# Optimization experiments

Hardware: AMD Instinct MI355X
Metric: run time of the kernel (lower is better)

## Reference

```python
import jax, jax.numpy as jnp
import numpy as np

B, S, D, H = 2, 4096, 512, 8
DK = D // H
LN_EPS = 1e-5


def setup_inputs() -> dict:
    key = jax.random.key(0)
    ks = jax.random.split(key, 12)
    lim = 1.0 / np.sqrt(D)
    inp = {
        "query": jax.random.normal(ks[0], (B, S, D), jnp.float32),
        "key_in": jax.random.normal(ks[1], (B, S, D), jnp.float32),
        "value": jax.random.normal(ks[2], (B, S, D), jnp.float32),
        # causal mask: positions with 0 are masked out (masked_fill(mask == 0, -1e9))
        "mask": jnp.broadcast_to(jnp.tril(jnp.ones((S, S), jnp.int32)), (B, S, S)),
        "Wq": jax.random.uniform(ks[3], (D, D), jnp.float32, -lim, lim),
        "bq": jnp.zeros((D,), jnp.float32),
        "Wk": jax.random.uniform(ks[4], (D, D), jnp.float32, -lim, lim),
        "bk": jnp.zeros((D,), jnp.float32),
        "Wv": jax.random.uniform(ks[5], (D, D), jnp.float32, -lim, lim),
        "bv": jnp.zeros((D,), jnp.float32),
        "Wo": jax.random.uniform(ks[6], (D, D), jnp.float32, -lim, lim),
        "bo": jnp.zeros((D,), jnp.float32),
        "ln_gamma": jnp.ones((D,), jnp.float32),
        "ln_beta": jnp.zeros((D,), jnp.float32),
    }
    return inp


def _split_heads(x):
    # [B, S, D] -> [B, H, S, DK]
    return x.reshape(B, S, H, DK).transpose(0, 2, 1, 3)


def reference(query, key_in, value, mask, Wq, bq, Wk, bk, Wv, bv, Wo, bo, ln_gamma, ln_beta):
    residual = query
    q = _split_heads(query @ Wq.T + bq)
    k = _split_heads(key_in @ Wk.T + bk)
    v = _split_heads(value @ Wv.T + bv)

    scores = jnp.einsum("bhqd,bhkd->bhqk", q, k) / jnp.sqrt(jnp.float32(DK))
    scores = jnp.where(mask[:, None, :, :] == 0, jnp.float32(-1e9), scores)
    attn = jax.nn.softmax(scores, axis=-1)  # dropout is identity in eval mode
    out = jnp.einsum("bhqk,bhkd->bhqd", attn, v)

    out = out.transpose(0, 2, 1, 3).reshape(B, S, D)
    out = out @ Wo.T + bo

    x = out + residual
    mu = jnp.mean(x, axis=-1, keepdims=True)
    var = jnp.mean(jnp.square(x - mu), axis=-1, keepdims=True)
    return (x - mu) * jax.lax.rsqrt(var + LN_EPS) * ln_gamma + ln_beta
```

## Files before the change

### kernel.cpp

```cpp
#include <hip/hip_runtime.h>
#include <hip/hip_bf16.h>

#define B_ 2
#define S_ 4096
#define D_ 512
#define H_ 8
#define DK_ 64

#define SCALE_LOG2 0.1803368801111244f

typedef short short8_t __attribute__((ext_vector_type(8)));
typedef short short4_t __attribute__((ext_vector_type(4)));
typedef float float4_t __attribute__((ext_vector_type(4)));

__device__ __forceinline__ unsigned cvtpk(float a, float b) {
    unsigned r;
    asm("v_cvt_pk_bf16_f32 %0, %1, %2" : "=v"(r) : "v"(a), "v"(b));
    return r;
}
union PU2 { unsigned u[2]; short4_t s4; };
union PU4 { unsigned u[4]; short8_t s8; };

#define MFMA32(a, b, c) __builtin_amdgcn_mfma_f32_16x16x32_bf16((a), (b), (c), 0, 0, 0)

#if __has_builtin(__builtin_amdgcn_mfma_f32_16x16x16bf16_1k)
__device__ __forceinline__ float4_t MFMA16(short4_t a, short4_t b, float4_t c) {
    return __builtin_amdgcn_mfma_f32_16x16x16bf16_1k(a, b, c, 0, 0, 0);
}
#else
__device__ __forceinline__ float4_t MFMA16(short4_t a, short4_t b, float4_t c) {
    asm volatile("v_mfma_f32_16x16x16_bf16 %0, %1, %2, %0" : "+v"(c) : "v"(a), "v"(b));
    return c;
}
#endif

__device__ __forceinline__ void gll16(const void* g, const void* l) {
    __builtin_amdgcn_global_load_lds(
        (__attribute__((address_space(1))) void*)(g),
        (__attribute__((address_space(3))) void*)(l), 16, 0, 0);
}

__global__ __launch_bounds__(256) void convert_all(
    const float* __restrict__ q, const float* __restrict__ k, const float* __restrict__ v,
    const float* __restrict__ Wq, const float* __restrict__ Wk,
    const float* __restrict__ Wv, const float* __restrict__ Wo,
    short* __restrict__ Xq, short* __restrict__ Xk, short* __restrict__ Xv,
    short* __restrict__ Wbf)
{
    const int XN = (B_ * S_ * D_) / 8;
    int gid = blockIdx.x * 256 + threadIdx.x;
    const float* src;
    short8_t* dst;
    int off;
    float sc = 1.f;
    if (gid < 3 * XN) {
        int z = gid >> 19;
        off = gid & (XN - 1);
        src = (z == 0) ? q : (z == 1) ? k : v;
        dst = (short8_t*)((z == 0) ? Xq : (z == 1) ? Xk : Xv);
    } else {
        int g2 = gid - 3 * XN;
        int z = g2 >> 15;
        off = g2 & 32767;
        src = (z == 0) ? Wq : (z == 1) ? Wk : (z == 2) ? Wv : Wo;
        dst = (short8_t*)(Wbf + z * (D_ * D_));
        if (z == 0) sc = SCALE_LOG2;
    }
    float4_t f0 = ((const float4_t*)src)[off * 2] * sc;
    float4_t f1 = ((const float4_t*)src)[off * 2 + 1] * sc;
    PU4 o;
    o.u[0] = cvtpk(f0[0], f0[1]);
    o.u[1] = cvtpk(f0[2], f0[3]);
    o.u[2] = cvtpk(f1[0], f1[1]);
    o.u[3] = cvtpk(f1[2], f1[3]);
    dst[off] = o.s8;
}

__global__ __launch_bounds__(256) void gemm_qkv(
    const short* __restrict__ Xq, const short* __restrict__ Xk, const short* __restrict__ Xv,
    const short* __restrict__ Wbf,
    const float* __restrict__ bq, const float* __restrict__ bk, const float* __restrict__ bv,
    short* __restrict__ Qs, short* __restrict__ Ks, short* __restrict__ Vt)
{
    __shared__ short sA[2][128 * 64];
    __shared__ short sB[2][128 * 64];

    const int z = blockIdx.z;
    const short* X    = (z == 0) ? Xq : (z == 1) ? Xk : Xv;
    const short* W    = Wbf + z * (D_ * D_);
    const float* bias = (z == 0) ? bq : (z == 1) ? bk : bv;

    const int col0 = blockIdx.x * 128, row0 = blockIdx.y * 128;
    const int tid = threadIdx.x, w = tid >> 6, l = tid & 63;
    const int lr = l & 15, lg = l >> 4;
    const int wm = w >> 1, wn = w & 1;
    const int srow = l >> 3, sch = l & 7;

    float4_t acc[4][4];
    #pragma unroll
    for (int i = 0; i < 4; i++)
        #pragma unroll
        for (int j = 0; j < 4; j++)
            acc[i][j] = (float4_t){0.f, 0.f, 0.f, 0.f};

    auto STAGE = [&](int k0, int bi) {
        #pragma unroll
        for (int rnd = 0; rnd < 4; rnd++) {
            int r = rnd * 32 + w * 8 + srow;
            gll16(X + (row0 + r) * D_ + k0 + (sch ^ (r & 7)) * 8, &sA[bi][(rnd * 32 + w * 8) * 64]);
            gll16(W + (col0 + r) * D_ + k0 + (sch ^ (r & 7)) * 8, &sB[bi][(rnd * 32 + w * 8) * 64]);
        }
    };

    STAGE(0, 0);
    for (int ks = 0; ks < 8; ks++) {
        int cur = ks & 1;
        if (ks < 7) {
            STAGE((ks + 1) * 64, cur ^ 1);
            asm volatile("s_waitcnt vmcnt(8)" ::: "memory");
        } else {
            asm volatile("s_waitcnt vmcnt(0)" ::: "memory");
        }
        __builtin_amdgcn_s_barrier();
        __builtin_amdgcn_sched_barrier(0);

        const short* pA = sA[cur];
        const short* pB = sB[cur];
        short8_t a[4], bb[4];
        #pragma unroll
        for (int kk = 0; kk < 2; kk++) {
            #pragma unroll
            for (int i = 0; i < 4; i++) {
                int rw = wm * 64 + i * 16 + lr;
                a[i] = *(const short8_t*)(&pA[rw * 64 + (((kk * 4 + lg) ^ (lr & 7)) * 8)]);
            }
            #pragma unroll
            for (int j = 0; j < 4; j++) {
                int rw = wn * 64 + j * 16 + lr;
                bb[j] = *(const short8_t*)(&pB[rw * 64 + (((kk * 4 + lg) ^ (lr & 7)) * 8)]);
            }
            if (z < 2) {
                #pragma unroll
                for (int i = 0; i < 4; i++)
                    #pragma unroll
                    for (int j = 0; j < 4; j++)
                        acc[i][j] = MFMA32(bb[j], a[i], acc[i][j]);
            } else {
                #pragma unroll
                for (int i = 0; i < 4; i++)
                    #pragma unroll
                    for (int j = 0; j < 4; j++)
                        acc[i][j] = MFMA32(a[i], bb[j], acc[i][j]);
            }
        }
        __builtin_amdgcn_s_barrier();
        __builtin_amdgcn_sched_barrier(0);
    }

    if (z < 2) {
        short* Out = (z == 0) ? Qs : Ks;
        #pragma unroll
        for (int j = 0; j < 4; j++) {
            int colb = col0 + wn * 64 + j * 16 + lg * 4;
            int h = colb >> 6, dk = colb & 63;
            float4_t b4 = *(const float4_t*)(bias + colb);
            if (z == 0) b4 *= SCALE_LOG2;
            #pragma unroll
            for (int i = 0; i < 4; i++) {
                int s = row0 + wm * 64 + i * 16 + lr;
                PU2 o;
                o.u[0] = cvtpk(acc[i][j][0] + b4[0], acc[i][j][1] + b4[1]);
                o.u[1] = cvtpk(acc[i][j][2] + b4[2], acc[i][j][3] + b4[3]);
                *(short4_t*)(Out + (((s >> 12) * H_ + h) * S_ + (s & 4095)) * 64 + dk) = o.s4;
            }
        }
    } else {
        #pragma unroll
        for (int j = 0; j < 4; j++) {
            int dkg = col0 + wn * 64 + j * 16 + lr;
            int h = dkg >> 6, dk = dkg & 63;
            float bv_ = bias[dkg];
            #pragma unroll
            for (int i = 0; i < 4; i++) {
                int s0 = row0 + wm * 64 + i * 16 + lg * 4;
                PU2 o;
                o.u[0] = cvtpk(acc[i][j][0] + bv_, acc[i][j][1] + bv_);
                o.u[1] = cvtpk(acc[i][j][2] + bv_, acc[i][j][3] + bv_);
                *(short4_t*)(Vt + (((s0 >> 12) * H_ + h) * 64 + dk) * S_ + (s0 & 4095)) = o.s4;
            }
        }
    }
}

__global__ __launch_bounds__(256) void attn_kernel(
    const short* __restrict__ Qs, const short* __restrict__ Ks,
    const short* __restrict__ Vt, short* __restrict__ Og)
{
    __shared__ float smem[8192];
    short* sKb = (short*)smem;
    short* sVb = (short*)smem + 8192;

    const int v = blockIdx.x;
    const int bh = (v & 7) * 2 + ((v >> 3) & 1);
    const int qt = 127 - (v >> 4);
    const int b = bh >> 3, h = bh & 7;
    const int tid = threadIdx.x, w = tid >> 6, l = tid & 63;
    const int lr = l & 15, lg = l >> 4;
    const int qbase = qt * 32;
    const int kvT = qt / 2 + 1;
    const short* Kb = Ks + bh * (S_ * 64);
    const short* Vb = Vt + bh * (64 * S_);
    const short* Qb = Qs + bh * (S_ * 64);
    const int srow = l >> 3, sch = l & 7;
    const short4_t ones = { (short)0x3F80, (short)0x3F80, (short)0x3F80, (short)0x3F80 };

    short8_t qf[2][2];
    #pragma unroll
    for (int qb = 0; qb < 2; qb++)
        #pragma unroll
        for (int kk = 0; kk < 2; kk++)
            qf[qb][kk] = *(const short8_t*)(Qb + (qbase + qb * 16 + lr) * 64 + kk * 32 + lg * 8);

    float m_run[2] = {-1e30f, -1e30f};
    float4_t Lacc[2];
    float4_t O[2][4];
    #pragma unroll
    for (int qb = 0; qb < 2; qb++) {
        Lacc[qb] = (float4_t){0.f, 0.f, 0.f, 0.f};
        #pragma unroll
        for (int nj = 0; nj < 4; nj++)
            O[qb][nj] = (float4_t){0.f, 0.f, 0.f, 0.f};
    }

    auto STAGE = [&](int t, int bi) {
        #pragma unroll
        for (int rnd = 0; rnd < 2; rnd++) {
            int r = rnd * 32 + w * 8 + srow;
            gll16(Kb + (t * 64 + r) * 64 + (sch ^ (r & 7)) * 8, sKb + bi * 4096 + (rnd * 32 + w * 8) * 64);
            gll16(Vb + r * S_ + t * 64 + (sch ^ (r & 7)) * 8,   sVb + bi * 4096 + (rnd * 32 + w * 8) * 64);
        }
    };

    STAGE(0, 0);
    for (int t = 0; t < kvT; t++) {
        int cur = t & 1;
        if (t + 1 < kvT) {
            STAGE(t + 1, cur ^ 1);
            asm volatile("s_waitcnt vmcnt(4)" ::: "memory");
        } else {
            asm volatile("s_waitcnt vmcnt(0)" ::: "memory");
        }
        __builtin_amdgcn_s_barrier();
        __builtin_amdgcn_sched_barrier(0);

        const int kv0 = t * 64 + w * 16;
        if (kv0 <= qbase + 16) {
            const short* K_ = sKb + cur * 4096;
            const short* V_ = sVb + cur * 4096;

            short8_t kf[2];
            #pragma unroll
            for (int kk = 0; kk < 2; kk++)
                kf[kk] = *(const short8_t*)(&K_[(w * 16 + lr) * 64 + (((kk * 4 + lg) ^ (lr & 7)) * 8)]);

            __builtin_amdgcn_s_setprio(1);
            float4_t st0 = (float4_t){0.f, 0.f, 0.f, 0.f}, st1 = st0;
            st0 = MFMA32(kf[0], qf[0][0], st0);
            st1 = MFMA32(kf[0], qf[1][0], st1);
            st0 = MFMA32(kf[1], qf[0][1], st0);
            st1 = MFMA32(kf[1], qf[1][1], st1);
            __builtin_amdgcn_s_setprio(0);

            const bool act0 = (kv0 <= qbase);
            const bool diag0 = (kv0 == qbase);
            const bool diag1 = (kv0 == qbase + 16);
            short4_t pb[2];

            #pragma unroll
            for (int qb = 0; qb < 2; qb++) {
                if (qb == 0 && !act0) continue;
                float4_t sx = qb ? st1 : st0;
                bool dg = qb ? diag1 : diag0;
                float mx = fmaxf(fmaxf(sx[0], sx[1]), fmaxf(sx[2], sx[3]));
                mx = fmaxf(mx, __shfl_xor(mx, 16));
                mx = fmaxf(mx, __shfl_xor(mx, 32));
                if (__any(mx > m_run[qb] + 8.f)) {
                    float mnew = fmaxf(m_run[qb], mx);
                    float al = __builtin_exp2f(m_run[qb] - mnew);
                    m_run[qb] = mnew;
                    #pragma unroll
                    for (int nj = 0; nj < 4; nj++) O[qb][nj] *= al;
                    Lacc[qb] *= al;
                }
                float e[4];
                #pragma unroll
                for (int r = 0; r < 4; r++)
                    e[r] = __builtin_exp2f(sx[r] - m_run[qb]);
                if (dg) {
                    #pragma unroll
                    for (int r = 0; r < 4; r++)
                        if (lg * 4 + r > lr) e[r] = 0.f;
                }
                PU2 pu;
                pu.u[0] = cvtpk(e[0], e[1]);
                pu.u[1] = cvtpk(e[2], e[3]);
                pb[qb] = pu.s4;
            }

            __builtin_amdgcn_s_setprio(1);
            if (act0) Lacc[0] = MFMA16(ones, pb[0], Lacc[0]);
            Lacc[1] = MFMA16(ones, pb[1], Lacc[1]);
            #pragma unroll
            for (int njd = 0; njd < 4; njd++) {
                short4_t va = *(const short4_t*)(
                    &V_[(njd * 16 + lr) * 64 + (((w * 2 + (lg >> 1)) ^ (lr & 7)) * 8) + (lg & 1) * 4]);
                if (act0) O[0][njd] = MFMA16(va, pb[0], O[0][njd]);
                O[1][njd] = MFMA16(va, pb[1], O[1][njd]);
            }
            __builtin_amdgcn_s_setprio(0);
        }
        __builtin_amdgcn_s_barrier();
        __builtin_amdgcn_sched_barrier(0);
    }

    float* sml = smem;
    if (lg == 0) {
        #pragma unroll
        for (int qb = 0; qb < 2; qb++) {
            sml[((w * 2 + qb) * 16 + lr) * 2 + 0] = m_run[qb];
            sml[((w * 2 + qb) * 16 + lr) * 2 + 1] = Lacc[qb][0];
        }
    }
    __syncthreads();
    float fac[2];
    #pragma unroll
    for (int qb = 0; qb < 2; qb++) {
        float mw[4], lw[4];
        #pragma unroll
        for (int ww = 0; ww < 4; ww++) {
            mw[ww] = sml[((ww * 2 + qb) * 16 + lr) * 2 + 0];
            lw[ww] = sml[((ww * 2 + qb) * 16 + lr) * 2 + 1];
        }
        float mmax = fmaxf(fmaxf(mw[0], mw[1]), fmaxf(mw[2], mw[3]));
        float lsum = 0.f;
        #pragma unroll
        for (int ww = 0; ww < 4; ww++) lsum += __builtin_exp2f(mw[ww] - mmax) * lw[ww];
        fac[qb] = __builtin_exp2f(m_run[qb] - mmax) / lsum;
    }
    __syncthreads();
    float* rg = smem + w * 2048;
    #pragma unroll
    for (int qb = 0; qb < 2; qb++) {
        #pragma unroll
        for (int njd = 0; njd < 4; njd++) {
            int row = qb * 16 + lr;
            int c = (njd * 4 + lg) ^ (lr & 7);
            float4_t val = O[qb][njd] * fac[qb];
            *(float4_t*)(rg + row * 64 + c * 4) = val;
        }
    }
    __syncthreads();
    {
        int qq = tid >> 3, a = tid & 7;
        int key = qq & 7;
        float4_t s0 = (float4_t){0.f, 0.f, 0.f, 0.f}, s1 = s0;
        #pragma unroll
        for (int ww = 0; ww < 4; ww++) {
            const float* r_ = smem + ww * 2048 + qq * 64;
            s0 += *(const float4_t*)(r_ + ((a * 2) ^ key) * 4);
            s1 += *(const float4_t*)(r_ + ((a * 2 + 1) ^ key) * 4);
        }
        PU4 o;
        o.u[0] = cvtpk(s0[0], s0[1]);
        o.u[1] = cvtpk(s0[2], s0[3]);
        o.u[2] = cvtpk(s1[0], s1[1]);
        o.u[3] = cvtpk(s1[2], s1[3]);
        *(short8_t*)(Og + (b * S_ + qbase + qq) * D_ + h * 64 + a * 8) = o.s8;
    }
}

__global__ __launch_bounds__(256) void gemm_oproj(
    const short* __restrict__ Ag, const short* __restrict__ Wbf,
    const float* __restrict__ bo, float* __restrict__ Og)
{
    __shared__ short sA[2][128 * 64];
    __shared__ short sB[2][128 * 64];

    const int col0 = blockIdx.x * 128, row0 = blockIdx.y * 128;
    const int tid = threadIdx.x, w = tid >> 6, l = tid & 63;
    const int lr = l & 15, lg = l >> 4;
    const int wm = w >> 1, wn = w & 1;
    const int srow = l >> 3, sch = l & 7;

    float4_t acc[4][4];
    #pragma unroll
    for (int i = 0; i < 4; i++)
        #pragma unroll
        for (int j = 0; j < 4; j++)
            acc[i][j] = (float4_t){0.f, 0.f, 0.f, 0.f};

    auto STAGE = [&](int k0, int bi) {
        #pragma unroll
        for (int rnd = 0; rnd < 4; rnd++) {
            int r = rnd * 32 + w * 8 + srow;
            gll16(Ag  + (row0 + r) * D_ + k0 + (sch ^ (r & 7)) * 8, &sA[bi][(rnd * 32 + w * 8) * 64]);
            gll16(Wbf + (col0 + r) * D_ + k0 + (sch ^ (r & 7)) * 8, &sB[bi][(rnd * 32 + w * 8) * 64]);
        }
    };

    STAGE(0, 0);
    for (int ks = 0; ks < 8; ks++) {
        int cur = ks & 1;
        if (ks < 7) {
            STAGE((ks + 1) * 64, cur ^ 1);
            asm volatile("s_waitcnt vmcnt(8)" ::: "memory");
        } else {
            asm volatile("s_waitcnt vmcnt(0)" ::: "memory");
        }
        __builtin_amdgcn_s_barrier();
        __builtin_amdgcn_sched_barrier(0);

        const short* pA = sA[cur];
        const short* pB = sB[cur];
        #pragma unroll
        for (int kk = 0; kk < 2; kk++) {
            short8_t a[4], bb[4];
            #pragma unroll
            for (int i = 0; i < 4; i++) {
                int rw = wm * 64 + i * 16 + lr;
                a[i] = *(const short8_t*)(&pA[rw * 64 + (((kk * 4 + lg) ^ (lr & 7)) * 8)]);
            }
            #pragma unroll
            for (int j = 0; j < 4; j++) {
                int rw = wn * 64 + j * 16 + lr;
                bb[j] = *(const short8_t*)(&pB[rw * 64 + (((kk * 4 + lg) ^ (lr & 7)) * 8)]);
            }
            #pragma unroll
            for (int i = 0; i < 4; i++)
                #pragma unroll
                for (int j = 0; j < 4; j++)
                    acc[i][j] = MFMA32(bb[j], a[i], acc[i][j]);
        }
        __builtin_amdgcn_s_barrier();
        __builtin_amdgcn_sched_barrier(0);
    }

    #pragma unroll
    for (int j = 0; j < 4; j++) {
        int colb = col0 + wn * 64 + j * 16 + lg * 4;
        float4_t b4 = *(const float4_t*)(bo + colb);
        #pragma unroll
        for (int i = 0; i < 4; i++) {
            int s = row0 + wm * 64 + i * 16 + lr;
            float4_t o4 = acc[i][j] + b4;
            *(float4_t*)(Og + s * D_ + colb) = o4;
        }
    }
}

__global__ __launch_bounds__(128) void ln_kernel(
    const float* __restrict__ Oin, const float* __restrict__ resid,
    const float* __restrict__ gamma, const float* __restrict__ beta,
    float* __restrict__ out)
{
    __shared__ float red[4];
    const int row = blockIdx.x, tid = threadIdx.x;
    float4_t o  = *(const float4_t*)(Oin   + row * 512 + tid * 4);
    float4_t rq = *(const float4_t*)(resid + row * 512 + tid * 4);
    float4_t x = o + rq;
    float s1 = x[0] + x[1] + x[2] + x[3];
    float s2 = x[0]*x[0] + x[1]*x[1] + x[2]*x[2] + x[3]*x[3];
    #pragma unroll
    for (int m = 1; m < 64; m <<= 1) {
        s1 += __shfl_xor(s1, m, 64);
        s2 += __shfl_xor(s2, m, 64);
    }
    const int wv = tid >> 6;
    if ((tid & 63) == 0) { red[wv * 2] = s1; red[wv * 2 + 1] = s2; }
    __syncthreads();
    s1 = red[0] + red[2];
    s2 = red[1] + red[3];
    float mu  = s1 * (1.f / 512.f);
    float var = s2 * (1.f / 512.f) - mu * mu;
    float rstd = rsqrtf(var + 1e-5f);
    float4_t g  = *(const float4_t*)(gamma + tid * 4);
    float4_t be = *(const float4_t*)(beta  + tid * 4);
    float4_t y;
    #pragma unroll
    for (int c = 0; c < 4; c++) y[c] = (x[c] - mu) * rstd * g[c] + be[c];
    *(float4_t*)(out + row * 512 + tid * 4) = y;
}

extern "C" void kernel_launch(void* const* d_in, const int* in_sizes, int n_in,
                              void* d_out, int out_size, void* d_ws, size_t ws_size,
                              hipStream_t stream) {
    const float* q     = (const float*)d_in[0];
    const float* kin   = (const float*)d_in[1];
    const float* vin   = (const float*)d_in[2];
    const float* Wq    = (const float*)d_in[4];
    const float* bq    = (const float*)d_in[5];
    const float* Wk    = (const float*)d_in[6];
    const float* bk    = (const float*)d_in[7];
    const float* Wv    = (const float*)d_in[8];
    const float* bv    = (const float*)d_in[9];
    const float* Wo    = (const float*)d_in[10];
    const float* bo    = (const float*)d_in[11];
    const float* gamma = (const float*)d_in[12];
    const float* beta  = (const float*)d_in[13];
    float* out = (float*)d_out;

    char* ws = (char*)d_ws;
    short* Wbf  = (short*)(ws);
    short* Xq   = (short*)(ws + 2097152);
    short* Xk   = (short*)(ws + 10485760);
    short* Xv   = (short*)(ws + 18874368);
    short* Qs   = (short*)(ws + 27262976);
    short* Ks   = (short*)(ws + 35651584);
    short* Vt   = (short*)(ws + 44040192);
    short* Attn = (short*)(ws + 18874368);
    float* Oprj = (float*)(ws + 2097152);

    convert_all<<<6656, 256, 0, stream>>>(q, kin, vin, Wq, Wk, Wv, Wo, Xq, Xk, Xv, Wbf);
    gemm_qkv<<<dim3(4, 64, 3), 256, 0, stream>>>(Xq, Xk, Xv, Wbf, bq, bk, bv, Qs, Ks, Vt);
    attn_kernel<<<2048, 256, 0, stream>>>(Qs, Ks, Vt, Attn);
    gemm_oproj<<<dim3(4, 64), 256, 0, stream>>>(Attn, Wbf + 3 * D_ * D_, bo, Oprj);
    ln_kernel<<<8192, 128, 0, stream>>>(Oprj, q, gamma, beta, out);
}
```

Before: 394.8 us.

## Double attention query tile to 64 rows per block to reuse staged K/V

Each attention block now handles 64 query rows (four 16-row sub-blocks) instead of 32, halving the grid to 1024 blocks and halving the K/V tile loads per query row. The causal check moves from per-tile skipping to diagonal handling only on the last KV tile, with each wave skipping the sub-blocks it does not need. The max shuffle reduction now runs only when a rescale may be needed. The epilogue reduction runs in two passes to fit shared memory. In exchange, register pressure rises from the larger O accumulators and there are fewer blocks to fill the GPU.

```diff
diff --git a/kernel.cpp b/kernel.cpp
--- a/kernel.cpp
+++ b/kernel.cpp
@@ -202,30 +202,30 @@
 
     const int v = blockIdx.x;
     const int bh = (v & 7) * 2 + ((v >> 3) & 1);
-    const int qt = 127 - (v >> 4);
+    const int qt = 63 - (v >> 4);
     const int b = bh >> 3, h = bh & 7;
     const int tid = threadIdx.x, w = tid >> 6, l = tid & 63;
     const int lr = l & 15, lg = l >> 4;
-    const int qbase = qt * 32;
-    const int kvT = qt / 2 + 1;
+    const int qbase = qt * 64;
+    const int kvT = qt + 1;
     const short* Kb = Ks + bh * (S_ * 64);
     const short* Vb = Vt + bh * (64 * S_);
     const short* Qb = Qs + bh * (S_ * 64);
     const int srow = l >> 3, sch = l & 7;
     const short4_t ones = { (short)0x3F80, (short)0x3F80, (short)0x3F80, (short)0x3F80 };
 
-    short8_t qf[2][2];
-    #pragma unroll
-    for (int qb = 0; qb < 2; qb++)
+    short8_t qf[4][2];
+    #pragma unroll
+    for (int qb = 0; qb < 4; qb++)
         #pragma unroll
         for (int kk = 0; kk < 2; kk++)
             qf[qb][kk] = *(const short8_t*)(Qb + (qbase + qb * 16 + lr) * 64 + kk * 32 + lg * 8);
 
-    float m_run[2] = {-1e30f, -1e30f};
-    float4_t Lacc[2];
-    float4_t O[2][4];
-    #pragma unroll
-    for (int qb = 0; qb < 2; qb++) {
+    float m_run[4] = {-1e30f, -1e30f, -1e30f, -1e30f};
+    float4_t Lacc[4];
+    float4_t O[4][4];
+    #pragma unroll
+    for (int qb = 0; qb < 4; qb++) {
         Lacc[qb] = (float4_t){0.f, 0.f, 0.f, 0.f};
         #pragma unroll
         for (int nj = 0; nj < 4; nj++)
@@ -253,72 +253,72 @@
         __builtin_amdgcn_s_barrier();
         __builtin_amdgcn_sched_barrier(0);
 
-        const int kv0 = t * 64 + w * 16;
-        if (kv0 <= qbase + 16) {
-            const short* K_ = sKb + cur * 4096;
-            const short* V_ = sVb + cur * 4096;
-
-            short8_t kf[2];
-            #pragma unroll
-            for (int kk = 0; kk < 2; kk++)
-                kf[kk] = *(const short8_t*)(&K_[(w * 16 + lr) * 64 + (((kk * 4 + lg) ^ (lr & 7)) * 8)]);
-
-            __builtin_amdgcn_s_setprio(1);
-            float4_t st0 = (float4_t){0.f, 0.f, 0.f, 0.f}, st1 = st0;
-            st0 = MFMA32(kf[0], qf[0][0], st0);
-            st1 = MFMA32(kf[0], qf[1][0], st1);
-            st0 = MFMA32(kf[1], qf[0][1], st0);
-            st1 = MFMA32(kf[1], qf[1][1], st1);
-            __builtin_amdgcn_s_setprio(0);
-
-            const bool act0 = (kv0 <= qbase);
-            const bool diag0 = (kv0 == qbase);
-            const bool diag1 = (kv0 == qbase + 16);
-            short4_t pb[2];
-
-            #pragma unroll
-            for (int qb = 0; qb < 2; qb++) {
-                if (qb == 0 && !act0) continue;
-                float4_t sx = qb ? st1 : st0;
-                bool dg = qb ? diag1 : diag0;
-                float mx = fmaxf(fmaxf(sx[0], sx[1]), fmaxf(sx[2], sx[3]));
+        const short* K_ = sKb + cur * 4096;
+        const short* V_ = sVb + cur * 4096;
+        const bool lastT = (t == kvT - 1);
+        const int qbS = lastT ? w : 0;
+
+        short8_t kf[2];
+        #pragma unroll
+        for (int kk = 0; kk < 2; kk++)
+            kf[kk] = *(const short8_t*)(&K_[(w * 16 + lr) * 64 + (((kk * 4 + lg) ^ (lr & 7)) * 8)]);
+
+        float4_t st[4];
+        __builtin_amdgcn_s_setprio(1);
+        #pragma unroll
+        for (int qb = 0; qb < 4; qb++) {
+            if (qb < qbS) continue;
+            st[qb] = (float4_t){0.f, 0.f, 0.f, 0.f};
+            st[qb] = MFMA32(kf[0], qf[qb][0], st[qb]);
+            st[qb] = MFMA32(kf[1], qf[qb][1], st[qb]);
+        }
+        __builtin_amdgcn_s_setprio(0);
+
+        short4_t pb[4];
+        #pragma unroll
+        for (int qb = 0; qb < 4; qb++) {
+            if (qb < qbS) continue;
+            float4_t sx = st[qb];
+            float mx = fmaxf(fmaxf(sx[0], sx[1]), fmaxf(sx[2], sx[3]));
+            if (__any(mx > m_run[qb] + 8.f)) {
                 mx = fmaxf(mx, __shfl_xor(mx, 16));
                 mx = fmaxf(mx, __shfl_xor(mx, 32));
-                if (__any(mx > m_run[qb] + 8.f)) {
-                    float mnew = fmaxf(m_run[qb], mx);
-                    float al = __builtin_exp2f(m_run[qb] - mnew);
-                    m_run[qb] = mnew;
-                    #pragma unroll
-                    for (int nj = 0; nj < 4; nj++) O[qb][nj] *= al;
-                    Lacc[qb] *= al;
-                }
-                float e[4];
+                float mnew = fmaxf(m_run[qb], mx);
+                float al = __builtin_exp2f(m_run[qb] - mnew);
+                m_run[qb] = mnew;
+                #pragma unroll
+                for (int nj = 0; nj < 4; nj++) O[qb][nj] *= al;
+                Lacc[qb] *= al;
+            }
+            float e[4];
+            #pragma unroll
+            for (int r = 0; r < 4; r++)
+                e[r] = __builtin_exp2f(sx[r] - m_run[qb]);
+            if (lastT && qb == w) {
                 #pragma unroll
                 for (int r = 0; r < 4; r++)
-                    e[r] = __builtin_exp2f(sx[r] - m_run[qb]);
-                if (dg) {
-                    #pragma unroll
-                    for (int r = 0; r < 4; r++)
-                        if (lg * 4 + r > lr) e[r] = 0.f;
-                }
-                PU2 pu;
-                pu.u[0] = cvtpk(e[0], e[1]);
-                pu.u[1] = cvtpk(e[2], e[3]);
-                pb[qb] = pu.s4;
-            }
-
-            __builtin_amdgcn_s_setprio(1);
-            if (act0) Lacc[0] = MFMA16(ones, pb[0], Lacc[0]);
-            Lacc[1] = MFMA16(ones, pb[1], Lacc[1]);
-            #pragma unroll
-            for (int njd = 0; njd < 4; njd++) {
-                short4_t va = *(const short4_t*)(
-                    &V_[(njd * 16 + lr) * 64 + (((w * 2 + (lg >> 1)) ^ (lr & 7)) * 8) + (lg & 1) * 4]);
-                if (act0) O[0][njd] = MFMA16(va, pb[0], O[0][njd]);
-                O[1][njd] = MFMA16(va, pb[1], O[1][njd]);
-            }
-            __builtin_amdgcn_s_setprio(0);
-        }
+                    if (lg * 4 + r > lr) e[r] = 0.f;
+            }
+            PU2 pu;
+            pu.u[0] = cvtpk(e[0], e[1]);
+            pu.u[1] = cvtpk(e[2], e[3]);
+            pb[qb] = pu.s4;
+        }
+
+        __builtin_amdgcn_s_setprio(1);
+        #pragma unroll
+        for (int qb = 0; qb < 4; qb++)
+            if (qb >= qbS) Lacc[qb] = MFMA16(ones, pb[qb], Lacc[qb]);
+        #pragma unroll
+        for (int njd = 0; njd < 4; njd++) {
+            short4_t va = *(const short4_t*)(
+                &V_[(njd * 16 + lr) * 64 + (((w * 2 + (lg >> 1)) ^ (lr & 7)) * 8) + (lg & 1) * 4]);
+            #pragma unroll
+            for (int qb = 0; qb < 4; qb++)
+                if (qb >= qbS) O[qb][njd] = MFMA16(va, pb[qb], O[qb][njd]);
+        }
+        __builtin_amdgcn_s_setprio(0);
+
         __builtin_amdgcn_s_barrier();
         __builtin_amdgcn_sched_barrier(0);
     }
@@ -326,20 +326,20 @@
     float* sml = smem;
     if (lg == 0) {
         #pragma unroll
-        for (int qb = 0; qb < 2; qb++) {
-            sml[((w * 2 + qb) * 16 + lr) * 2 + 0] = m_run[qb];
-            sml[((w * 2 + qb) * 16 + lr) * 2 + 1] = Lacc[qb][0];
+        for (int qb = 0; qb < 4; qb++) {
+            sml[((w * 4 + qb) * 16 + lr) * 2 + 0] = m_run[qb];
+            sml[((w * 4 + qb) * 16 + lr) * 2 + 1] = Lacc[qb][0];
         }
     }
     __syncthreads();
-    float fac[2];
-    #pragma unroll
-    for (int qb = 0; qb < 2; qb++) {
+    float fac[4];
+    #pragma unroll
+    for (int qb = 0; qb < 4; qb++) {
         float mw[4], lw[4];
         #pragma unroll
         for (int ww = 0; ww < 4; ww++) {
-            mw[ww] = sml[((ww * 2 + qb) * 16 + lr) * 2 + 0];
-            lw[ww] = sml[((ww * 2 + qb) * 16 + lr) * 2 + 1];
+            mw[ww] = sml[((ww * 4 + qb) * 16 + lr) * 2 + 0];
+            lw[ww] = sml[((ww * 4 + qb) * 16 + lr) * 2 + 1];
         }
         float mmax = fmaxf(fmaxf(mw[0], mw[1]), fmaxf(mw[2], mw[3]));
         float lsum = 0.f;
@@ -348,34 +348,38 @@
         fac[qb] = __builtin_exp2f(m_run[qb] - mmax) / lsum;
     }
     __syncthreads();
-    float* rg = smem + w * 2048;
-    #pragma unroll
-    for (int qb = 0; qb < 2; qb++) {
-        #pragma unroll
-        for (int njd = 0; njd < 4; njd++) {
-            int row = qb * 16 + lr;
-            int c = (njd * 4 + lg) ^ (lr & 7);
-            float4_t val = O[qb][njd] * fac[qb];
-            *(float4_t*)(rg + row * 64 + c * 4) = val;
-        }
-    }
-    __syncthreads();
-    {
-        int qq = tid >> 3, a = tid & 7;
-        int key = qq & 7;
-        float4_t s0 = (float4_t){0.f, 0.f, 0.f, 0.f}, s1 = s0;
-        #pragma unroll
-        for (int ww = 0; ww < 4; ww++) {
-            const float* r_ = smem + ww * 2048 + qq * 64;
-            s0 += *(const float4_t*)(r_ + ((a * 2) ^ key) * 4);
-            s1 += *(const float4_t*)(r_ + ((a * 2 + 1) ^ key) * 4);
-        }
-        PU4 o;
-        o.u[0] = cvtpk(s0[0], s0[1]);
-        o.u[1] = cvtpk(s0[2], s0[3]);
-        o.u[2] = cvtpk(s1[0], s1[1]);
-        o.u[3] = cvtpk(s1[2], s1[3]);
-        *(short8_t*)(Og + (b * S_ + qbase + qq) * D_ + h * 64 + a * 8) = o.s8;
+    #pragma unroll
+    for (int pass = 0; pass < 2; pass++) {
+        float* rg = smem + w * 2048;
+        #pragma unroll
+        for (int q2 = 0; q2 < 2; q2++) {
+            int qb = pass * 2 + q2;
+            #pragma unroll
+            for (int njd = 0; njd < 4; njd++) {
+                int row = q2 * 16 + lr;
+                int c = (njd * 4 + lg) ^ (lr & 7);
+                *(float4_t*)(rg + row * 64 + c * 4) = O[qb][njd] * fac[qb];
+            }
+        }
+        __syncthreads();
+        {
+            int qq = tid >> 3, a = tid & 7;
+            int key = qq & 7;
+            float4_t s0 = (float4_t){0.f, 0.f, 0.f, 0.f}, s1 = s0;
+            #pragma unroll
+            for (int ww = 0; ww < 4; ww++) {
+                const float* r_ = smem + ww * 2048 + qq * 64;
+                s0 += *(const float4_t*)(r_ + ((a * 2) ^ key) * 4);
+                s1 += *(const float4_t*)(r_ + ((a * 2 + 1) ^ key) * 4);
+            }
+            PU4 o;
+            o.u[0] = cvtpk(s0[0], s0[1]);
+            o.u[1] = cvtpk(s0[2], s0[3]);
+            o.u[2] = cvtpk(s1[0], s1[1]);
+            o.u[3] = cvtpk(s1[2], s1[3]);
+            *(short8_t*)(Og + (b * S_ + qbase + pass * 32 + qq) * D_ + h * 64 + a * 8) = o.s8;
+        }
+        if (pass == 0) __syncthreads();
     }
 }
 
@@ -522,7 +526,7 @@
 
     convert_all<<<6656, 256, 0, stream>>>(q, kin, vin, Wq, Wk, Wv, Wo, Xq, Xk, Xv, Wbf);
     gemm_qkv<<<dim3(4, 64, 3), 256, 0, stream>>>(Xq, Xk, Xv, Wbf, bq, bk, bv, Qs, Ks, Vt);
-    attn_kernel<<<2048, 256, 0, stream>>>(Qs, Ks, Vt, Attn);
+    attn_kernel<<<1024, 256, 0, stream>>>(Qs, Ks, Vt, Attn);
     gemm_oproj<<<dim3(4, 64), 256, 0, stream>>>(Attn, Wbf + 3 * D_ * D_, bo, Oprj);
     ln_kernel<<<8192, 128, 0, stream>>>(Oprj, q, gamma, beta, out);
 }
```

Measured after the change: 379.4 us. 1.04x faster.
